# Kernel tuning notes

Hardware: AMD Instinct MI355X
Metric: run time of the kernel (lower is better)

Reference implementation:

```python
import jax, jax.numpy as jnp
import numpy as np

HIDDEN = 4096
N_HEADS = 32
N_KV_HEADS = 8
HEAD_DIM = HIDDEN // N_HEADS  # 128
N_KV_GROUPS = N_HEADS // N_KV_HEADS  # 4
SEQ = 2048
BSZ = 1
ROPE_THETA = 10000.0


def _rope_cos_sin(seqlen, head_dim, dtype):
    # freqs_cis = polar(1, outer(t, theta^{-2i/d})) -> cos/sin tables [S, hd/2]
    inv_freq = 1.0 / (ROPE_THETA ** (jnp.arange(0, head_dim, 2, dtype=jnp.float32) / head_dim))
    t = jnp.arange(seqlen, dtype=jnp.float32)
    freqs = jnp.outer(t, inv_freq)  # [S, hd/2]
    return jnp.cos(freqs).astype(dtype), jnp.sin(freqs).astype(dtype)


def _apply_rotary(x, cos, sin):
    # x: [B, S, H, hd]. Torch code pairs (x[:hd/2], x[hd/2:]) as (real, imag):
    # out = concat(x1*cos - x2*sin, x1*sin + x2*cos)
    half = x.shape[-1] // 2
    x1, x2 = x[..., :half], x[..., half:]
    c = cos[None, :, None, :]  # [1, S, 1, hd/2]
    s = sin[None, :, None, :]
    return jnp.concatenate([x1 * c - x2 * s, x1 * s + x2 * c], axis=-1)


def setup_inputs() -> dict:
    key = jax.random.key(0)
    k1, k2, k3 = jax.random.split(key, 3)
    hidden_states = jax.random.normal(k1, (BSZ, SEQ, HIDDEN), dtype=jnp.float32)
    w_qkv = jax.random.normal(k2, (HIDDEN, (N_HEADS + 2 * N_KV_HEADS) * HEAD_DIM), dtype=jnp.float32) * 0.02
    w_o = jax.random.normal(k3, (HIDDEN, HIDDEN), dtype=jnp.float32) * 0.02
    # HF-style additive causal mask [1, 1, S, S]
    causal = jnp.tril(jnp.ones((SEQ, SEQ), dtype=bool))
    attention_mask = jnp.where(causal, 0.0, -1e9).astype(jnp.float32)[None, None]
    return {"hidden_states": hidden_states, "w_qkv": w_qkv, "w_o": w_o,
            "attention_mask": attention_mask}


def reference(hidden_states, w_qkv, w_o, attention_mask):
    bsz, seqlen, _ = hidden_states.shape
    # fused (dequantized) QKV projection
    xqkv = jnp.einsum('bsh,hd->bsd', hidden_states, w_qkv)
    xqkv = xqkv.reshape(bsz, seqlen, N_HEADS + 2 * N_KV_HEADS, HEAD_DIM)
    xq = xqkv[:, :, :N_HEADS]                      # [B, S, 32, 128]
    xk = xqkv[:, :, N_HEADS:N_HEADS + N_KV_HEADS]  # [B, S, 8, 128]
    xv = xqkv[:, :, -N_KV_HEADS:]                  # [B, S, 8, 128]

    cos, sin = _rope_cos_sin(seqlen, HEAD_DIM, hidden_states.dtype)
    xq = _apply_rotary(xq, cos, sin)
    xk = _apply_rotary(xk, cos, sin)

    # GQA: repeat_interleave kv heads along head dim
    keys = jnp.repeat(xk, N_KV_GROUPS, axis=2)    # [B, S, 32, 128]
    values = jnp.repeat(xv, N_KV_GROUPS, axis=2)

    q = xq.transpose(0, 2, 1, 3)   # [B, H, S, D]
    k = keys.transpose(0, 2, 1, 3)
    v = values.transpose(0, 2, 1, 3)

    scores = jnp.einsum('bhqd,bhkd->bhqk', q, k) / np.sqrt(HEAD_DIM)
    scores = scores + attention_mask
    probs = jax.nn.softmax(scores.astype(jnp.float32), axis=-1).astype(q.dtype)
    out = jnp.einsum('bhqk,bhkd->bhqd', probs, v)
    attention_weight = out.transpose(0, 2, 1, 3).reshape(bsz, seqlen, -1)
    attn_output = jnp.einsum('bsh,ho->bso', attention_weight, w_o)
    return attn_output
```

## Files before the change

kernel.cpp:

```cpp
#include <hip/hip_runtime.h>
#include <stdint.h>

typedef unsigned short u16;
typedef __bf16 bf8 __attribute__((ext_vector_type(8)));
typedef float f32x4 __attribute__((ext_vector_type(4)));

#define SEQ 2048
#define HIDDEN 4096
#define DQKV 6144
#define HD 128

#define GLOAD_LDS16(g, l)                                                            \
    __builtin_amdgcn_global_load_lds((const __attribute__((address_space(1))) void*)(g), \
                                     (__attribute__((address_space(3))) void*)(l), 16, 0, 0)

__device__ __forceinline__ u16 f2bf(float f) {
    union { float f; unsigned u; } v{f};
    unsigned r = (v.u + 0x7fff + ((v.u >> 16) & 1)) >> 16;
    return (u16)r;
}
__device__ __forceinline__ float bf2f(u16 b) {
    union { unsigned u; float f; } v;
    v.u = ((unsigned)b) << 16;
    return v.f;
}


__global__ void convert_bf16_kernel(const float* __restrict__ in, u16* __restrict__ out) {
    int i = (blockIdx.x * 256 + threadIdx.x) * 4;
    float4 v = *(const float4*)(in + i);
    u16 o[4] = {f2bf(v.x), f2bf(v.y), f2bf(v.z), f2bf(v.w)};
    *(uint2*)(out + i) = *(uint2*)o;
}

__global__ void transpose_w_kernel(const float* __restrict__ in, u16* __restrict__ out, int K, int N) {
    __shared__ u16 tile[64][65];
    int tn = N >> 6;
    int bk = blockIdx.x / tn, bn = blockIdx.x % tn;
    int k0 = bk * 64, n0 = bn * 64;
    int c = threadIdx.x & 63, r0 = threadIdx.x >> 6;
#pragma unroll
    for (int r = r0; r < 64; r += 4)
        tile[r][c] = f2bf(in[(size_t)(k0 + r) * N + n0 + c]);
    __syncthreads();
#pragma unroll
    for (int r = r0; r < 64; r += 4)
        out[(size_t)(n0 + r) * K + k0 + c] = tile[c][r];
}

__global__ void rope_kernel(u16* __restrict__ x) {
    const int row = blockIdx.x / 10, hg = blockIdx.x % 10;
    const int head = hg * 4 + (threadIdx.x >> 6), j = threadIdx.x & 63;
    u16* p = x + (size_t)row * DQKV + head * HD + j;
    float x1 = bf2f(p[0]), x2 = bf2f(p[64]);
    float inv = exp2f(-(float)j * 0.20762050593045952f);
    float s, c;
    sincosf((float)row * inv, &s, &c);
    p[0] = f2bf(x1 * c - x2 * s);
    p[64] = f2bf(x1 * s + x2 * c);
}

__global__ void transpose_v_kernel(const u16* __restrict__ xqkv, u16* __restrict__ vt) {
    __shared__ u16 tile[64][65];
    int h = blockIdx.x >> 6;
    int t = blockIdx.x & 63;
    int s0 = (t >> 1) * 64, d0 = (t & 1) * 64;
    int c = threadIdx.x & 63, r0 = threadIdx.x >> 6;
    const u16* src = xqkv + (40 + h) * HD + d0;
#pragma unroll
    for (int r = r0; r < 64; r += 4)
        tile[r][c] = src[(size_t)(s0 + r) * DQKV + c];
    __syncthreads();
    u16* dst = vt + ((size_t)h * HD + d0) * SEQ + s0;
#pragma unroll
    for (int r = r0; r < 64; r += 4)
        dst[(size_t)r * SEQ + c] = tile[c][r];
}

template <int BM, int BN, int MODE>
__global__ __launch_bounds__(512, 2) void gemm8p_kernel(const u16* __restrict__ A,
                                                        const u16* __restrict__ BT,
                                                        u16* __restrict__ Cbf,
                                                        float* __restrict__ Cf) {
    constexpr int WM = BM / 32;
    constexpr int WN = BN / 64;
    constexpr int MP = WM / 4;
    constexpr int NLA = BM / 64, NLB = BN / 64, NL = NLA + NLB;
    constexpr int NBN = ((MODE == 0) ? DQKV : HIDDEN) / BN;
    constexpr int CSTR = (MODE == 0) ? DQKV : HIDDEN;
    constexpr int NT = 64;
    __shared__ __align__(16) u16 lds[2][(BM + BN) * 64];

    const int tid = threadIdx.x;
    const int w = tid >> 6, l = tid & 63, l15 = l & 15, q4 = l >> 4;
    const int wm = w >> 2, wn = w & 3;
    const int bm = blockIdx.x / NBN, bn = blockIdx.x % NBN;

    const int srow = tid >> 3;
    const int scol = ((tid & 7) ^ ((tid >> 3) & 7)) << 4;
    const char* spA[NLA];
    const char* spB[NLB];
#pragma unroll
    for (int L = 0; L < NLA; ++L)
        spA[L] = (const char*)(A + (size_t)(bm * BM + L * 64 + srow) * 4096) + scol;
#pragma unroll
    for (int L = 0; L < NLB; ++L)
        spB[L] = (const char*)(BT + (size_t)(bn * BN + L * 64 + srow) * 4096) + scol;

#define STG_A(L, tt, b) GLOAD_LDS16(spA[L] + (size_t)(tt) * 128, &lds[b][(L) * 4096 + w * 512])
#define STG_B(L, tt, b) GLOAD_LDS16(spB[L] + (size_t)(tt) * 128, &lds[b][BM * 64 + (L) * 4096 + w * 512])

#pragma unroll
    for (int L = 0; L < NLA; ++L) STG_A(L, 0, 0);
#pragma unroll
    for (int L = 0; L < NLB; ++L) STG_B(L, 0, 0);
#pragma unroll
    for (int L = 0; L < NLA; ++L) STG_A(L, 1, 1);
#pragma unroll
    for (int L = 0; L < NLB; ++L) STG_B(L, 1, 1);
    if constexpr (NL == 7) asm volatile("s_waitcnt vmcnt(7)" ::: "memory");
    else                   asm volatile("s_waitcnt vmcnt(6)" ::: "memory");
    asm volatile("s_barrier" ::: "memory");

    const int c0x = (q4 * 16) ^ ((l15 & 7) << 4);
    const int c1x = (64 + q4 * 16) ^ ((l15 & 7) << 4);

    f32x4 acc[WM][WN] = {};
    bf8 breg[WN][2];

#pragma unroll 1
    for (int t = 0; t < NT; ++t) {
        const int cur = t & 1;
        const char* ldsA = (const char*)&lds[cur][0];
        const char* ldsB = ldsA + BM * 128;
#pragma unroll
        for (int p = 0; p < 4; ++p) {
            if (p == 1 && t < NT - 2) {
#pragma unroll
                for (int L = 0; L < NLB; ++L) STG_B(L, t + 2, cur);
            }
            if constexpr (BM == 256) {
                if (p == 2 && t < NT - 2) {
                    STG_A(0, t + 2, cur);
                    STG_A(2, t + 2, cur);
                }
            }
            bf8 areg[MP][2];
#pragma unroll
            for (int j = 0; j < MP; ++j) {
                const char* rp = ldsA + (wm * (BM / 2) + (p * MP + j) * 16 + l15) * 128;
                areg[j][0] = *(const bf8*)(rp + c0x);
                areg[j][1] = *(const bf8*)(rp + c1x);
            }
            if (p == 0) {
#pragma unroll
                for (int nf = 0; nf < WN; ++nf) {
                    const char* rp = ldsB + (wn * (WN * 16) + nf * 16 + l15) * 128;
                    breg[nf][0] = *(const bf8*)(rp + c0x);
                    breg[nf][1] = *(const bf8*)(rp + c1x);
                }
            }
            asm volatile("s_barrier" ::: "memory");
            asm volatile("s_waitcnt lgkmcnt(0)" ::: "memory");
            __builtin_amdgcn_s_setprio(1);
#pragma unroll
            for (int j = 0; j < MP; ++j)
#pragma unroll
                for (int nf = 0; nf < WN; ++nf)
#pragma unroll
                    for (int ks = 0; ks < 2; ++ks)
                        acc[p * MP + j][nf] = __builtin_amdgcn_mfma_f32_16x16x32_bf16(
                            areg[j][ks], breg[nf][ks], acc[p * MP + j][nf], 0, 0, 0);
            __builtin_amdgcn_s_setprio(0);
            asm volatile("s_barrier" ::: "memory");
        }
        if (t < NT - 2) {
            if constexpr (BM == 256) { STG_A(1, t + 2, cur); STG_A(3, t + 2, cur); }
            else                     { STG_A(0, t + 2, cur); STG_A(1, t + 2, cur); }
            if constexpr (NL == 7) asm volatile("s_waitcnt vmcnt(7)" ::: "memory");
            else                   asm volatile("s_waitcnt vmcnt(6)" ::: "memory");
        } else if (t == NT - 2) {
            asm volatile("s_waitcnt vmcnt(0)" ::: "memory");
        }
        asm volatile("s_barrier" ::: "memory");
    }
#undef STG_A
#undef STG_B

    const int rowb = bm * BM + wm * (BM / 2);
    const int colb = bn * BN + wn * (WN * 16);
#pragma unroll
    for (int mf = 0; mf < WM; ++mf)
#pragma unroll
        for (int nf = 0; nf < WN; ++nf)
#pragma unroll
            for (int r = 0; r < 4; ++r) {
                const int row = rowb + mf * 16 + q4 * 4 + r;
                const int col = colb + nf * 16 + l15;
                if constexpr (MODE == 0)
                    Cbf[(size_t)row * CSTR + col] = f2bf(acc[mf][nf][r]);
                else
                    Cf[(size_t)row * CSTR + col] = acc[mf][nf][r];
            }
}

#define PSTR 72
__global__ __launch_bounds__(256) void attn_kernel(const u16* __restrict__ xqkv,
                                                   const u16* __restrict__ vt,
                                                   u16* __restrict__ aw) {
    __shared__ __align__(16) u16 sm[16384 + 128 * PSTR];
    const int tid = threadIdx.x, w = tid >> 6, l = tid & 63, l15 = l & 15, q4 = l >> 4;
    const int qh = blockIdx.x & 31;
    const int qslot = blockIdx.x >> 5;
    const int qt = (qslot < 8) ? qslot : 23 - qslot;
    const int kh = qh >> 2;

    {
        const u16* gq = xqkv + (size_t)(qt * 128 + (l >> 2)) * DQKV + qh * HD + w * 32 + (l & 3) * 8;
#pragma unroll
        for (int i = 0; i < 8; ++i)
            GLOAD_LDS16(gq + (size_t)i * 16 * DQKV, &sm[w * 4096 + i * 512]);
    }
    __syncthreads();
    bf8 qf[4][2];
#pragma unroll
    for (int ks = 0; ks < 4; ++ks)
#pragma unroll
        for (int mt = 0; mt < 2; ++mt)
            qf[ks][mt] = *(const bf8*)&sm[ks * 4096 + (w * 32 + mt * 16 + l15) * 32 + q4 * 8];
    __syncthreads();

    f32x4 O[2][8] = {};
    float plrow[2][4] = {};

    u16* ldsK = sm;
    u16* ldsV = sm + 8192;
    u16* ldsP = sm + 16384;
    const int nkt = 2 * qt + 2;
    const float cs = 0.12751744f;

    const u16* gk_base = xqkv + (32 + kh) * HD + w * 32 + (l & 3) * 8;
    const u16* gv_base = vt + (size_t)kh * HD * SEQ + (size_t)((w & 1) * 64 + (l >> 2)) * SEQ + (w >> 1) * 32 + (l & 3) * 8;

    for (int kt = 0; kt < nkt; ++kt) {
        {
            const u16* gk = gk_base + (size_t)(kt * 64 + (l >> 2)) * DQKV;
#pragma unroll
            for (int i = 0; i < 4; ++i)
                GLOAD_LDS16(gk + (size_t)i * 16 * DQKV, ldsK + w * 2048 + i * 512);
        }
        {
            const u16* gv = gv_base + kt * 64;
#pragma unroll
            for (int i = 0; i < 4; ++i)
                GLOAD_LDS16(gv + (size_t)i * 16 * SEQ, ldsV + (w >> 1) * 4096 + (w & 1) * 2048 + i * 512);
        }
        __syncthreads();

        f32x4 S[2][4] = {};
#pragma unroll
        for (int ks = 0; ks < 4; ++ks) {
            bf8 kf[4];
#pragma unroll
            for (int nt = 0; nt < 4; ++nt)
                kf[nt] = *(const bf8*)&ldsK[ks * 2048 + (nt * 16 + l15) * 32 + q4 * 8];
#pragma unroll
            for (int mt = 0; mt < 2; ++mt)
#pragma unroll
                for (int nt = 0; nt < 4; ++nt)
                    S[mt][nt] = __builtin_amdgcn_mfma_f32_16x16x32_bf16(qf[ks][mt], kf[nt], S[mt][nt], 0, 0, 0);
        }

        const bool domask = (kt >= 2 * qt);
#pragma unroll
        for (int mt = 0; mt < 2; ++mt)
#pragma unroll
            for (int r = 0; r < 4; ++r) {
                const int row = qt * 128 + w * 32 + mt * 16 + q4 * 4 + r;
#pragma unroll
                for (int nt = 0; nt < 4; ++nt) {
                    float t = S[mt][nt][r] * cs;
                    if (domask && (kt * 64 + nt * 16 + l15 > row)) t = -1e30f;
                    float p = exp2f(t);
                    plrow[mt][r] += p;
                    ldsP[(w * 32 + mt * 16 + q4 * 4 + r) * PSTR + nt * 16 + l15] = f2bf(p);
                }
            }

#pragma unroll
        for (int pk = 0; pk < 2; ++pk) {
            bf8 pf[2], vf[8];
#pragma unroll
            for (int mt = 0; mt < 2; ++mt)
                pf[mt] = *(const bf8*)&ldsP[(w * 32 + mt * 16 + l15) * PSTR + pk * 32 + q4 * 8];
#pragma unroll
            for (int nt = 0; nt < 8; ++nt)
                vf[nt] = *(const bf8*)&ldsV[pk * 4096 + (nt * 16 + l15) * 32 + q4 * 8];
#pragma unroll
            for (int mt = 0; mt < 2; ++mt)
#pragma unroll
                for (int nt = 0; nt < 8; ++nt)
                    O[mt][nt] = __builtin_amdgcn_mfma_f32_16x16x32_bf16(pf[mt], vf[nt], O[mt][nt], 0, 0, 0);
        }
        __syncthreads();
    }

#pragma unroll
    for (int mt = 0; mt < 2; ++mt)
#pragma unroll
        for (int r = 0; r < 4; ++r) {
            float ls = plrow[mt][r];
#pragma unroll
            for (int off = 1; off <= 8; off <<= 1)
                ls += __shfl_xor(ls, off, 64);
            const float linv = 1.0f / ls;
            const int row = qt * 128 + w * 32 + mt * 16 + q4 * 4 + r;
#pragma unroll
            for (int nt = 0; nt < 8; ++nt)
                aw[(size_t)row * 4096 + qh * HD + nt * 16 + l15] = f2bf(O[mt][nt][r] * linv);
        }
}


extern "C" void kernel_launch(void* const* d_in, const int* in_sizes, int n_in,
                              void* d_out, int out_size, void* d_ws, size_t ws_size,
                              hipStream_t stream) {
    const float* hs = (const float*)d_in[0];
    const float* wqkv = (const float*)d_in[1];
    const float* wo = (const float*)d_in[2];
    float* out = (float*)d_out;

    char* ws = (char*)d_ws;
    const size_t oHbf = 0;
    const size_t oWqkvT = oHbf + (size_t)SEQ * HIDDEN * 2;
    const size_t oWoT = oWqkvT + (size_t)DQKV * HIDDEN * 2;
    const size_t oXQKV = oWoT + (size_t)HIDDEN * HIDDEN * 2;
    const size_t oVT = oXQKV + (size_t)SEQ * DQKV * 2;
    const size_t oAW = oVT + (size_t)8 * HD * SEQ * 2;
    const size_t total = oAW + (size_t)SEQ * HIDDEN * 2;
    if (ws_size < total) return;

    u16* Hbf = (u16*)(ws + oHbf);
    u16* WqkvT = (u16*)(ws + oWqkvT);
    u16* WoT = (u16*)(ws + oWoT);
    u16* XQKV = (u16*)(ws + oXQKV);
    u16* VT = (u16*)(ws + oVT);
    u16* AW = (u16*)(ws + oAW);

    convert_bf16_kernel<<<(SEQ * HIDDEN) / 1024, 256, 0, stream>>>(hs, Hbf);
    transpose_w_kernel<<<(HIDDEN / 64) * (DQKV / 64), 256, 0, stream>>>(wqkv, WqkvT, HIDDEN, DQKV);
    transpose_w_kernel<<<(HIDDEN / 64) * (HIDDEN / 64), 256, 0, stream>>>(wo, WoT, HIDDEN, HIDDEN);
    gemm8p_kernel<256, 192, 0><<<8 * 32, 512, 0, stream>>>(Hbf, WqkvT, XQKV, nullptr);
    rope_kernel<<<SEQ * 10, 256, 0, stream>>>(XQKV);
    transpose_v_kernel<<<8 * 64, 256, 0, stream>>>(XQKV, VT);
    attn_kernel<<<512, 256, 0, stream>>>(XQKV, VT, AW);
    gemm8p_kernel<128, 256, 1><<<16 * 16, 512, 0, stream>>>(AW, WoT, nullptr, out);
}
```

Before: 519.3 us.

## Switch GEMMs to 32x32x16 MFMA with new warp layout and simpler pipeline

Rewrites the GEMM inner loop to use 32x32x16 bf16 MFMA instead of 16x16x32. Warps are rearranged as 4x2 with 64-row by WNF*32-column tiles, which reduces LDS reads per FLOP. The staging schedule is simplified to issue all next-tile loads after compute, with two barriers per K-tile. The output GEMM tile also changes from 128x256 to 256x128. The risks are less overlap of global loads with compute and higher register pressure under launch bounds of 512 threads with 2 blocks.

Measured after the change: 538.3 us. 3.7% more time.

```diff
diff --git a/kernel.cpp b/kernel.cpp
--- a/kernel.cpp
+++ b/kernel.cpp
@@ -4,6 +4,7 @@
 typedef unsigned short u16;
 typedef __bf16 bf8 __attribute__((ext_vector_type(8)));
 typedef float f32x4 __attribute__((ext_vector_type(4)));
+typedef float f32x16 __attribute__((ext_vector_type(16)));
 
 #define SEQ 2048
 #define HIDDEN 4096
@@ -78,13 +79,11 @@
 }
 
 template <int BM, int BN, int MODE>
-__global__ __launch_bounds__(512, 2) void gemm8p_kernel(const u16* __restrict__ A,
+__global__ __launch_bounds__(512, 2) void gemm32_kernel(const u16* __restrict__ A,
                                                         const u16* __restrict__ BT,
                                                         u16* __restrict__ Cbf,
                                                         float* __restrict__ Cf) {
-    constexpr int WM = BM / 32;
-    constexpr int WN = BN / 64;
-    constexpr int MP = WM / 4;
+    constexpr int WNF = BN / 64;
     constexpr int NLA = BM / 64, NLB = BN / 64, NL = NLA + NLB;
     constexpr int NBN = ((MODE == 0) ? DQKV : HIDDEN) / BN;
     constexpr int CSTR = (MODE == 0) ? DQKV : HIDDEN;
@@ -92,8 +91,8 @@
     __shared__ __align__(16) u16 lds[2][(BM + BN) * 64];
 
     const int tid = threadIdx.x;
-    const int w = tid >> 6, l = tid & 63, l15 = l & 15, q4 = l >> 4;
-    const int wm = w >> 2, wn = w & 3;
+    const int w = tid >> 6, l = tid & 63, l31 = l & 31, hi = l >> 5;
+    const int wm = w >> 1, wn = w & 1;
     const int bm = blockIdx.x / NBN, bn = blockIdx.x % NBN;
 
     const int srow = tid >> 3;
@@ -122,85 +121,98 @@
     else                   asm volatile("s_waitcnt vmcnt(6)" ::: "memory");
     asm volatile("s_barrier" ::: "memory");
 
-    const int c0x = (q4 * 16) ^ ((l15 & 7) << 4);
-    const int c1x = (64 + q4 * 16) ^ ((l15 & 7) << 4);
-
-    f32x4 acc[WM][WN] = {};
-    bf8 breg[WN][2];
+    const int cx = ((hi ^ (l & 7)) << 4);
+    int aoff[2], boff[WNF];
+#pragma unroll
+    for (int mf = 0; mf < 2; ++mf)
+        aoff[mf] = (wm * 64 + mf * 32 + l31) * 128;
+#pragma unroll
+    for (int nf = 0; nf < WNF; ++nf)
+        boff[nf] = BM * 128 + (wn * (WNF * 32) + nf * 32 + l31) * 128;
+
+    f32x16 acc[2][WNF] = {};
 
 #pragma unroll 1
-    for (int t = 0; t < NT; ++t) {
-        const int cur = t & 1;
-        const char* ldsA = (const char*)&lds[cur][0];
-        const char* ldsB = ldsA + BM * 128;
-#pragma unroll
-        for (int p = 0; p < 4; ++p) {
-            if (p == 1 && t < NT - 2) {
-#pragma unroll
-                for (int L = 0; L < NLB; ++L) STG_B(L, t + 2, cur);
-            }
-            if constexpr (BM == 256) {
-                if (p == 2 && t < NT - 2) {
-                    STG_A(0, t + 2, cur);
-                    STG_A(2, t + 2, cur);
-                }
-            }
-            bf8 areg[MP][2];
-#pragma unroll
-            for (int j = 0; j < MP; ++j) {
-                const char* rp = ldsA + (wm * (BM / 2) + (p * MP + j) * 16 + l15) * 128;
-                areg[j][0] = *(const bf8*)(rp + c0x);
-                areg[j][1] = *(const bf8*)(rp + c1x);
-            }
-            if (p == 0) {
-#pragma unroll
-                for (int nf = 0; nf < WN; ++nf) {
-                    const char* rp = ldsB + (wn * (WN * 16) + nf * 16 + l15) * 128;
-                    breg[nf][0] = *(const bf8*)(rp + c0x);
-                    breg[nf][1] = *(const bf8*)(rp + c1x);
-                }
+    for (int tt = 0; tt < NT; tt += 2) {
+#pragma unroll
+        for (int half = 0; half < 2; ++half) {
+            const int t = tt + half;
+            const char* base = (const char*)&lds[half][0];
+
+            bf8 a0[2][2], b0[WNF][2];
+#pragma unroll
+            for (int mf = 0; mf < 2; ++mf)
+#pragma unroll
+                for (int kk = 0; kk < 2; ++kk)
+                    a0[mf][kk] = *(const bf8*)(base + aoff[mf] + ((kk << 5) ^ cx));
+#pragma unroll
+            for (int nf = 0; nf < WNF; ++nf)
+#pragma unroll
+                for (int kk = 0; kk < 2; ++kk)
+                    b0[nf][kk] = *(const bf8*)(base + boff[nf] + ((kk << 5) ^ cx));
+
+            __builtin_amdgcn_s_setprio(1);
+#pragma unroll
+            for (int mf = 0; mf < 2; ++mf)
+#pragma unroll
+                for (int nf = 0; nf < WNF; ++nf)
+#pragma unroll
+                    for (int kk = 0; kk < 2; ++kk)
+                        acc[mf][nf] = __builtin_amdgcn_mfma_f32_32x32x16_bf16(
+                            a0[mf][kk], b0[nf][kk], acc[mf][nf], 0, 0, 0);
+
+            bf8 a1[2][2], b1[WNF][2];
+#pragma unroll
+            for (int mf = 0; mf < 2; ++mf)
+#pragma unroll
+                for (int kk = 0; kk < 2; ++kk)
+                    a1[mf][kk] = *(const bf8*)(base + aoff[mf] + (((2 + kk) << 5) ^ cx));
+#pragma unroll
+            for (int nf = 0; nf < WNF; ++nf)
+#pragma unroll
+                for (int kk = 0; kk < 2; ++kk)
+                    b1[nf][kk] = *(const bf8*)(base + boff[nf] + (((2 + kk) << 5) ^ cx));
+#pragma unroll
+            for (int mf = 0; mf < 2; ++mf)
+#pragma unroll
+                for (int nf = 0; nf < WNF; ++nf)
+#pragma unroll
+                    for (int kk = 0; kk < 2; ++kk)
+                        acc[mf][nf] = __builtin_amdgcn_mfma_f32_32x32x16_bf16(
+                            a1[mf][kk], b1[nf][kk], acc[mf][nf], 0, 0, 0);
+            __builtin_amdgcn_s_setprio(0);
+
+            asm volatile("s_barrier" ::: "memory");
+            if (t < NT - 2) {
+#pragma unroll
+                for (int L = 0; L < NLA; ++L) STG_A(L, t + 2, half);
+#pragma unroll
+                for (int L = 0; L < NLB; ++L) STG_B(L, t + 2, half);
+                if constexpr (NL == 7) asm volatile("s_waitcnt vmcnt(7)" ::: "memory");
+                else                   asm volatile("s_waitcnt vmcnt(6)" ::: "memory");
+            } else if (t == NT - 2) {
+                asm volatile("s_waitcnt vmcnt(0)" ::: "memory");
             }
             asm volatile("s_barrier" ::: "memory");
-            asm volatile("s_waitcnt lgkmcnt(0)" ::: "memory");
-            __builtin_amdgcn_s_setprio(1);
-#pragma unroll
-            for (int j = 0; j < MP; ++j)
-#pragma unroll
-                for (int nf = 0; nf < WN; ++nf)
-#pragma unroll
-                    for (int ks = 0; ks < 2; ++ks)
-                        acc[p * MP + j][nf] = __builtin_amdgcn_mfma_f32_16x16x32_bf16(
-                            areg[j][ks], breg[nf][ks], acc[p * MP + j][nf], 0, 0, 0);
-            __builtin_amdgcn_s_setprio(0);
-            asm volatile("s_barrier" ::: "memory");
-        }
-        if (t < NT - 2) {
-            if constexpr (BM == 256) { STG_A(1, t + 2, cur); STG_A(3, t + 2, cur); }
-            else                     { STG_A(0, t + 2, cur); STG_A(1, t + 2, cur); }
-            if constexpr (NL == 7) asm volatile("s_waitcnt vmcnt(7)" ::: "memory");
-            else                   asm volatile("s_waitcnt vmcnt(6)" ::: "memory");
-        } else if (t == NT - 2) {
-            asm volatile("s_waitcnt vmcnt(0)" ::: "memory");
-        }
-        asm volatile("s_barrier" ::: "memory");
+        }
     }
 #undef STG_A
 #undef STG_B
 
-    const int rowb = bm * BM + wm * (BM / 2);
-    const int colb = bn * BN + wn * (WN * 16);
-#pragma unroll
-    for (int mf = 0; mf < WM; ++mf)
-#pragma unroll
-        for (int nf = 0; nf < WN; ++nf)
-#pragma unroll
-            for (int r = 0; r < 4; ++r) {
-                const int row = rowb + mf * 16 + q4 * 4 + r;
-                const int col = colb + nf * 16 + l15;
+    const int rowb = bm * BM + wm * 64 + hi * 4;
+    const int colb = bn * BN + wn * (WNF * 32) + l31;
+#pragma unroll
+    for (int mf = 0; mf < 2; ++mf)
+#pragma unroll
+        for (int nf = 0; nf < WNF; ++nf)
+#pragma unroll
+            for (int reg = 0; reg < 16; ++reg) {
+                const int row = rowb + mf * 32 + (reg & 3) + 8 * (reg >> 2);
+                const int col = colb + nf * 32;
                 if constexpr (MODE == 0)
-                    Cbf[(size_t)row * CSTR + col] = f2bf(acc[mf][nf][r]);
+                    Cbf[(size_t)row * CSTR + col] = f2bf(acc[mf][nf][reg]);
                 else
-                    Cf[(size_t)row * CSTR + col] = acc[mf][nf][r];
+                    Cf[(size_t)row * CSTR + col] = acc[mf][nf][reg];
             }
 }
 
@@ -350,9 +362,9 @@
     convert_bf16_kernel<<<(SEQ * HIDDEN) / 1024, 256, 0, stream>>>(hs, Hbf);
     transpose_w_kernel<<<(HIDDEN / 64) * (DQKV / 64), 256, 0, stream>>>(wqkv, WqkvT, HIDDEN, DQKV);
     transpose_w_kernel<<<(HIDDEN / 64) * (HIDDEN / 64), 256, 0, stream>>>(wo, WoT, HIDDEN, HIDDEN);
-    gemm8p_kernel<256, 192, 0><<<8 * 32, 512, 0, stream>>>(Hbf, WqkvT, XQKV, nullptr);
+    gemm32_kernel<256, 192, 0><<<256, 512, 0, stream>>>(Hbf, WqkvT, XQKV, nullptr);
     rope_kernel<<<SEQ * 10, 256, 0, stream>>>(XQKV);
     transpose_v_kernel<<<8 * 64, 256, 0, stream>>>(XQKV, VT);
     attn_kernel<<<512, 256, 0, stream>>>(XQKV, VT, AW);
-    gemm8p_kernel<128, 256, 1><<<16 * 16, 512, 0, stream>>>(AW, WoT, nullptr, out);
-}
+    gemm32_kernel<256, 128, 1><<<256, 512, 0, stream>>>(AW, WoT, nullptr, out);
+}
```

## Software-pipeline LDS fragment loads in GEMM and retile output projection

Applied to the files above, without the earlier changes.

Restructures the GEMM main loop so A fragments for the next 32-row chunk are read from LDS while the current chunk's MFMAs run. The per-phase barriers are removed, and all global-to-LDS staging for tile t+2 is issued after a single barrier at the end of each k-step. The output-projection GEMM changes from 128x256 to 256x128 tiles so both GEMMs use the 256-row path. The schedule trades the staggered mid-iteration prefetch for fewer barriers and double-buffered A registers, which may raise register pressure and can expose global-load latency at the end of each iteration.

Result: slower. 541.8 us (+4.3%).

```diff
diff --git a/kernel.cpp b/kernel.cpp
--- a/kernel.cpp
+++ b/kernel.cpp
@@ -78,13 +78,13 @@
 }
 
 template <int BM, int BN, int MODE>
-__global__ __launch_bounds__(512, 2) void gemm8p_kernel(const u16* __restrict__ A,
-                                                        const u16* __restrict__ BT,
-                                                        u16* __restrict__ Cbf,
-                                                        float* __restrict__ Cf) {
+__global__ __launch_bounds__(512, 2) void gemmp_kernel(const u16* __restrict__ A,
+                                                       const u16* __restrict__ BT,
+                                                       u16* __restrict__ Cbf,
+                                                       float* __restrict__ Cf) {
     constexpr int WM = BM / 32;
     constexpr int WN = BN / 64;
-    constexpr int MP = WM / 4;
+    constexpr int NC = WM / 2;
     constexpr int NLA = BM / 64, NLB = BN / 64, NL = NLA + NLB;
     constexpr int NBN = ((MODE == 0) ? DQKV : HIDDEN) / BN;
     constexpr int CSTR = (MODE == 0) ? DQKV : HIDDEN;
@@ -123,67 +123,69 @@
     asm volatile("s_barrier" ::: "memory");
 
     const int c0x = (q4 * 16) ^ ((l15 & 7) << 4);
-    const int c1x = (64 + q4 * 16) ^ ((l15 & 7) << 4);
+    const int c1x = c0x ^ 64;
 
     f32x4 acc[WM][WN] = {};
     bf8 breg[WN][2];
+    bf8 areg[2][2][2];
+
+#define LD_B(b)                                                              \
+    do {                                                                     \
+        _Pragma("unroll") for (int nf = 0; nf < WN; ++nf) {                  \
+            const char* rp = (const char*)&lds[b][BM * 64]                   \
+                             + (wn * (WN * 16) + nf * 16 + l15) * 128;       \
+            breg[nf][0] = *(const bf8*)(rp + c0x);                           \
+            breg[nf][1] = *(const bf8*)(rp + c1x);                           \
+        }                                                                    \
+    } while (0)
+#define LD_APAIR(cc, b)                                                      \
+    do {                                                                     \
+        _Pragma("unroll") for (int j = 0; j < 2; ++j) {                      \
+            const char* rp = (const char*)&lds[b][0]                         \
+                             + (wm * (BM / 2) + ((cc) * 2 + j) * 16 + l15) * 128; \
+            areg[(cc) & 1][j][0] = *(const bf8*)(rp + c0x);                  \
+            areg[(cc) & 1][j][1] = *(const bf8*)(rp + c1x);                  \
+        }                                                                    \
+    } while (0)
+
+    LD_B(0);
+    LD_APAIR(0, 0);
 
 #pragma unroll 1
     for (int t = 0; t < NT; ++t) {
         const int cur = t & 1;
-        const char* ldsA = (const char*)&lds[cur][0];
-        const char* ldsB = ldsA + BM * 128;
-#pragma unroll
-        for (int p = 0; p < 4; ++p) {
-            if (p == 1 && t < NT - 2) {
-#pragma unroll
-                for (int L = 0; L < NLB; ++L) STG_B(L, t + 2, cur);
-            }
-            if constexpr (BM == 256) {
-                if (p == 2 && t < NT - 2) {
-                    STG_A(0, t + 2, cur);
-                    STG_A(2, t + 2, cur);
-                }
-            }
-            bf8 areg[MP][2];
-#pragma unroll
-            for (int j = 0; j < MP; ++j) {
-                const char* rp = ldsA + (wm * (BM / 2) + (p * MP + j) * 16 + l15) * 128;
-                areg[j][0] = *(const bf8*)(rp + c0x);
-                areg[j][1] = *(const bf8*)(rp + c1x);
-            }
-            if (p == 0) {
-#pragma unroll
-                for (int nf = 0; nf < WN; ++nf) {
-                    const char* rp = ldsB + (wn * (WN * 16) + nf * 16 + l15) * 128;
-                    breg[nf][0] = *(const bf8*)(rp + c0x);
-                    breg[nf][1] = *(const bf8*)(rp + c1x);
-                }
-            }
-            asm volatile("s_barrier" ::: "memory");
-            asm volatile("s_waitcnt lgkmcnt(0)" ::: "memory");
+#pragma unroll
+        for (int c = 0; c < NC; ++c) {
+            if (c < NC - 1) LD_APAIR(c + 1, cur);
             __builtin_amdgcn_s_setprio(1);
 #pragma unroll
-            for (int j = 0; j < MP; ++j)
+            for (int j = 0; j < 2; ++j)
 #pragma unroll
                 for (int nf = 0; nf < WN; ++nf)
 #pragma unroll
                     for (int ks = 0; ks < 2; ++ks)
-                        acc[p * MP + j][nf] = __builtin_amdgcn_mfma_f32_16x16x32_bf16(
-                            areg[j][ks], breg[nf][ks], acc[p * MP + j][nf], 0, 0, 0);
+                        acc[c * 2 + j][nf] = __builtin_amdgcn_mfma_f32_16x16x32_bf16(
+                            areg[c & 1][j][ks], breg[nf][ks], acc[c * 2 + j][nf], 0, 0, 0);
             __builtin_amdgcn_s_setprio(0);
-            asm volatile("s_barrier" ::: "memory");
-        }
+        }
+        if (t == NT - 1) break;
+        asm volatile("s_barrier" ::: "memory");
         if (t < NT - 2) {
-            if constexpr (BM == 256) { STG_A(1, t + 2, cur); STG_A(3, t + 2, cur); }
-            else                     { STG_A(0, t + 2, cur); STG_A(1, t + 2, cur); }
+#pragma unroll
+            for (int L = 0; L < NLA; ++L) STG_A(L, t + 2, cur);
+#pragma unroll
+            for (int L = 0; L < NLB; ++L) STG_B(L, t + 2, cur);
             if constexpr (NL == 7) asm volatile("s_waitcnt vmcnt(7)" ::: "memory");
             else                   asm volatile("s_waitcnt vmcnt(6)" ::: "memory");
-        } else if (t == NT - 2) {
+        } else {
             asm volatile("s_waitcnt vmcnt(0)" ::: "memory");
         }
         asm volatile("s_barrier" ::: "memory");
+        LD_B(cur ^ 1);
+        LD_APAIR(0, cur ^ 1);
     }
+#undef LD_B
+#undef LD_APAIR
 #undef STG_A
 #undef STG_B
 
@@ -350,9 +352,9 @@
     convert_bf16_kernel<<<(SEQ * HIDDEN) / 1024, 256, 0, stream>>>(hs, Hbf);
     transpose_w_kernel<<<(HIDDEN / 64) * (DQKV / 64), 256, 0, stream>>>(wqkv, WqkvT, HIDDEN, DQKV);
     transpose_w_kernel<<<(HIDDEN / 64) * (HIDDEN / 64), 256, 0, stream>>>(wo, WoT, HIDDEN, HIDDEN);
-    gemm8p_kernel<256, 192, 0><<<8 * 32, 512, 0, stream>>>(Hbf, WqkvT, XQKV, nullptr);
+    gemmp_kernel<256, 192, 0><<<256, 512, 0, stream>>>(Hbf, WqkvT, XQKV, nullptr);
     rope_kernel<<<SEQ * 10, 256, 0, stream>>>(XQKV);
     transpose_v_kernel<<<8 * 64, 256, 0, stream>>>(XQKV, VT);
     attn_kernel<<<512, 256, 0, stream>>>(XQKV, VT, AW);
-    gemm8p_kernel<128, 256, 1><<<16 * 16, 512, 0, stream>>>(AW, WoT, nullptr, out);
-}
+    gemmp_kernel<256, 128, 1><<<256, 512, 0, stream>>>(AW, WoT, nullptr, out);
+}
```
